# Kernel tuning notes

Measured on AMD Instinct MI355X. Metric: run time of the kernel, lower is better.

Reference implementation:

```python
import jax, jax.numpy as jnp
import numpy as np

NT = 256
T = 8192

def setup_inputs() -> dict:
    key = jax.random.key(0)
    k1, k2, k3, k4, k5 = jax.random.split(key, 5)
    emit = jax.random.normal(k1, (T, NT), dtype=jnp.float32)
    y = jax.random.randint(k2, (T,), 0, NT, dtype=jnp.int64)
    trans = jax.random.normal(k3, (NT, NT), dtype=jnp.float32)
    BOS = jax.random.normal(k4, (NT,), dtype=jnp.float32)
    EOS = jax.random.normal(k5, (NT,), dtype=jnp.float32)
    return {"emit": emit, "y": y, "trans": trans, "BOS": BOS, "EOS": EOS}

def _log_z(emit, trans, BOS):
    # alpha recurrence: alpha_new[j] = emit_i[j] + logsumexp_k(trans[k, j] + alpha[k])
    alpha0 = BOS + emit[0]
    def step(alpha, emit_i):
        alpha_new = emit_i + jax.nn.logsumexp(trans + alpha[:, None], axis=0)
        return alpha_new, None
    alpha, _ = jax.lax.scan(step, alpha0, emit[1:])
    return jax.nn.logsumexp(alpha)

def _gold_score(emit, y, trans, BOS, EOS):
    T_ = emit.shape[0]
    idx = jnp.arange(T_ - 1)
    s = BOS[y[0]]
    # faithful to original: emit[i, y[i]] for i in 0..T-2, plus trans[y[i], y[i+1]]
    s = s + jnp.sum(trans[y[:-1], y[1:]]) + jnp.sum(emit[idx, y[:-1]])
    s = s + EOS[y[-1]] + emit[-1, y[-1]]
    return s

def reference(emit, y, trans, BOS, EOS):
    logZ = _log_z(emit, trans, BOS)
    return logZ - _gold_score(emit, y, trans, BOS, EOS)
```

## Files before the change

kernel.cpp:

```cpp
#include <hip/hip_runtime.h>
#include <hip/hip_fp16.h>

#define TLEN 8192
#define NTS  256
#define CLEN 32
#define NCH  256
#define SLOT2 66048

typedef __bf16 bf16x8 __attribute__((ext_vector_type(8)));
typedef float  f32x4  __attribute__((ext_vector_type(4)));
union U128 { uint4 u; bf16x8 v; };
union U64  { uint2 u; long l; };

__device__ __forceinline__ unsigned f2bfu(float x) {
    unsigned u = __float_as_uint(x);
    return (u + 0x7fffu + ((u >> 16) & 1u)) >> 16;
}
__device__ __forceinline__ unsigned pk2(float lo, float hi) {
    return f2bfu(lo) | (f2bfu(hi) << 16);
}
__device__ __forceinline__ float bf2f(unsigned short h) {
    return __uint_as_float(((unsigned)h) << 16);
}
__device__ __forceinline__ unsigned pk4bf8(float a, float b, float c, float d) {
    int r = __builtin_amdgcn_cvt_pk_bf8_f32(a, b, 0, false);
    r = __builtin_amdgcn_cvt_pk_bf8_f32(c, d, r, true);
    return (unsigned)r;
}
__device__ __forceinline__ float dot8(uint4 a, const float* uq) {
    return bf2f((unsigned short)(a.x & 0xffffu)) * uq[0]
         + bf2f((unsigned short)(a.x >> 16))     * uq[1]
         + bf2f((unsigned short)(a.y & 0xffffu)) * uq[2]
         + bf2f((unsigned short)(a.y >> 16))     * uq[3]
         + bf2f((unsigned short)(a.z & 0xffffu)) * uq[4]
         + bf2f((unsigned short)(a.z >> 16))     * uq[5]
         + bf2f((unsigned short)(a.w & 0xffffu)) * uq[6]
         + bf2f((unsigned short)(a.w >> 16))     * uq[7];
}

__global__ __launch_bounds__(256, 2) void crf_phase1(
        const float* __restrict__ emit, const float* __restrict__ trans,
        char* __restrict__ outX) {
    __shared__ alignas(16) char qt8[65536];
    __shared__ alignas(16) char scr[4][1280];
    __shared__ alignas(16) float eld[2][NTS];

    const int t    = threadIdx.x;
    const int lane = t & 63;
    const int w    = t >> 6;
    const int gl   = lane >> 4;
    const int ln15 = lane & 15;
    const int c    = blockIdx.x >> 1;
    const int h    = blockIdx.x & 1;
    const int istart = (c == 0) ? 1 : CLEN * c;
    const int iend   = CLEN * c + CLEN;

    {
        const int ln = t & 15;
        for (int gk = 0; gk < 32; gk++) {
            float v[8];
            #pragma unroll
            for (int e = 0; e < 8; e++) v[e] = __expf(trans[(gk * 8 + e) * NTS + t]);
            uint2 u;
            u.x = pk4bf8(v[0], v[1], v[2], v[3]);
            u.y = pk4bf8(v[4], v[5], v[6], v[7]);
            const int p = (gk + 4 * ln + (ln >> 2)) & 31;
            *(uint2*)(qt8 + t * 256 + p * 8) = u;
        }
    }
    eld[istart & 1][t] = __expf(emit[istart * NTS + t]);

    int aoff[8];
    #pragma unroll
    for (int kf = 0; kf < 8; kf++) {
        const int p = (4 * kf + gl + 4 * ln15 + (ln15 >> 2)) & 31;
        aoff[kf] = ln15 * 256 + p * 8;
    }

    uint2 Bf[8][2];
    #pragma unroll
    for (int kf = 0; kf < 8; kf++)
        #pragma unroll
        for (int cb = 0; cb < 2; cb++) {
            uint2 bu; bu.x = 0u; bu.y = 0u;
            const int r_glob = 128 * h + 32 * w + cb * 16 + ln15;
            if ((r_glob >> 3) == kf * 4 + gl) {
                const int e = r_glob & 7;
                if (e < 4) bu.x = 0x3Cu << (8 * e);
                else       bu.y = 0x3Cu << (8 * (e - 4));
            }
            Bf[kf][cb] = bu;
        }
    float rs[2] = {0.f, 0.f};
    __syncthreads();

    char* const mysc = &scr[w][0];
    for (int i = istart; i < iend; ++i) {
        float enext = 0.f;
        if (i + 1 < iend) enext = emit[(i + 1) * NTS + t];

        f32x4 Cacc[16][2];
        #pragma unroll
        for (int jb = 0; jb < 16; jb++)
            #pragma unroll
            for (int cb = 0; cb < 2; cb++) Cacc[jb][cb] = f32x4{0.f, 0.f, 0.f, 0.f};

        #pragma unroll
        for (int jb = 0; jb < 16; jb++) {
            #pragma unroll
            for (int kf = 0; kf < 8; kf++) {
                U64 a; a.u = *(const uint2*)(qt8 + (aoff[kf] + jb * 4096));
                #pragma unroll
                for (int cb = 0; cb < 2; cb++) {
                    U64 b; b.u = Bf[kf][cb];
                    Cacc[jb][cb] = __builtin_amdgcn_mfma_f32_16x16x32_bf8_bf8(
                        a.l, b.l, Cacc[jb][cb], 0, 0, 0);
                }
            }
        }

        #pragma unroll
        for (int jb = 0; jb < 16; jb++) {
            float4 ev = *(const float4*)&eld[i & 1][jb * 16 + gl * 4];
            #pragma unroll
            for (int cb = 0; cb < 2; cb++) {
                Cacc[jb][cb][0] *= ev.x; Cacc[jb][cb][1] *= ev.y;
                Cacc[jb][cb][2] *= ev.z; Cacc[jb][cb][3] *= ev.w;
            }
        }
        float rn[2];
        #pragma unroll
        for (int cb = 0; cb < 2; cb++) {
            float m0 = Cacc[0][cb][0];
            #pragma unroll
            for (int jb = 0; jb < 16; jb++)
                #pragma unroll
                for (int rg = 0; rg < 4; rg++) m0 = fmaxf(m0, Cacc[jb][cb][rg]);
            m0 = fmaxf(m0, __shfl_xor(m0, 16));
            m0 = fmaxf(m0, __shfl_xor(m0, 32));
            rn[cb] = 1.0f / m0;
            rs[cb] += __logf(m0);
        }

        if (i == iend - 1) {
            __syncthreads();
            #pragma unroll
            for (int jb = 0; jb < 16; jb++)
                #pragma unroll
                for (int cb = 0; cb < 2; cb++) {
                    int rsl = w * 32 + cb * 16 + ln15;
                    #pragma unroll
                    for (int rg = 0; rg < 4; rg++) {
                        int j = jb * 16 + gl * 4 + rg;
                        *(unsigned short*)(qt8 + ((j * 128 + rsl) << 1)) =
                            (unsigned short)f2bfu(Cacc[jb][cb][rg] * rn[cb]);
                    }
                }
            __syncthreads();
            char* SO = outX + (size_t)(2 * c + h) * SLOT2;
            #pragma unroll
            for (int q = 0; q < 16; q++)
                *(uint4*)(SO + q * 4096 + t * 16) =
                    *(const uint4*)(qt8 + q * 4096 + t * 16);
            if (lane < 16) {
                #pragma unroll
                for (int cb = 0; cb < 2; cb++) {
                    int rsl = w * 32 + cb * 16 + lane;
                    *(float*)(SO + 65536 + rsl * 4) = rs[cb];
                }
            }
        } else {
            #pragma unroll
            for (int kf = 0; kf < 8; kf++) {
                #pragma unroll
                for (int jbb = 0; jbb < 2; jbb++) {
                    const int jb = 2 * kf + jbb;
                    #pragma unroll
                    for (int cb = 0; cb < 2; cb++) {
                        const int col = cb * 16 + ln15;
                        unsigned pk = pk4bf8(Cacc[jb][cb][0] * rn[cb],
                                             Cacc[jb][cb][1] * rn[cb],
                                             Cacc[jb][cb][2] * rn[cb],
                                             Cacc[jb][cb][3] * rn[cb]);
                        *(unsigned*)(mysc + col * 40 + jbb * 16 + gl * 4) = pk;
                    }
                }
                asm volatile("s_waitcnt lgkmcnt(0)" ::: "memory");
                __builtin_amdgcn_sched_barrier(0);
                #pragma unroll
                for (int cb = 0; cb < 2; cb++) {
                    const int col = cb * 16 + ln15;
                    Bf[kf][cb] = *(const uint2*)(mysc + col * 40 + gl * 8);
                }
                asm volatile("s_waitcnt lgkmcnt(0)" ::: "memory");
                __builtin_amdgcn_sched_barrier(0);
            }
            eld[(i + 1) & 1][t] = __expf(enext);
            __syncthreads();
        }
    }
}

__device__ __forceinline__ void combine_body(
        const char* __restrict__ inb, char* __restrict__ outb,
        int p, int h, char* qt, unsigned (*scr)[512],
        float* efac, float* smax,
        int t, int lane, int w, int gl, int ln15) {
    const char* SL0 = inb + (size_t)(4 * p + 2) * SLOT2;
    const char* SL1 = inb + (size_t)(4 * p + 3) * SLOT2;
    const char* SE  = inb + (size_t)(4 * p + h) * SLOT2;
    char* SO = outb + (size_t)(2 * p + h) * SLOT2;

    float sv = *(const float*)(((t < 128) ? SL0 : SL1) + 65536 + (t & 127) * 4);
    float m = sv;
    #pragma unroll
    for (int off = 32; off; off >>= 1) m = fmaxf(m, __shfl_xor(m, off));
    if (lane == 0) smax[w] = m;
    __syncthreads();
    const float sigma = fmaxf(fmaxf(smax[0], smax[1]), fmaxf(smax[2], smax[3]));
    efac[t] = __expf(sv - sigma);
    __syncthreads();

    for (int it = 0; it < 32; it++) {
        int off = it * 2048 + t * 8;
        int j = off >> 8, k = off & 255;
        const char* src = (k < 128) ? (SL0 + (size_t)(j * 128 + k) * 2)
                                    : (SL1 + (size_t)(j * 128 + (k - 128)) * 2);
        uint4 d = *(const uint4*)src;
        float4 e0 = *(const float4*)&efac[k];
        float4 e1 = *(const float4*)&efac[k + 4];
        float ef[8] = {e0.x, e0.y, e0.z, e0.w, e1.x, e1.y, e1.z, e1.w};
        unsigned wds[4] = {d.x, d.y, d.z, d.w};
        unsigned outw[4];
        #pragma unroll
        for (int wi = 0; wi < 4; wi++) {
            float lo = bf2f((unsigned short)(wds[wi] & 0xffffu)) * ef[2 * wi];
            float hi = bf2f((unsigned short)(wds[wi] >> 16)) * ef[2 * wi + 1];
            outw[wi] = pk2(lo, hi);
        }
        uint4 o; o.x = outw[0]; o.y = outw[1]; o.z = outw[2]; o.w = outw[3];
        *(uint4*)(qt + ((j * 512 + k * 2) ^ ((j & 7) << 4))) = o;
    }

    bf16x8 Bf[8][2];
    #pragma unroll
    for (int kf = 0; kf < 8; kf++) {
        #pragma unroll
        for (int p2 = 0; p2 < 2; p2++) {
            int kk = p2 * 16 + (lane >> 2);
            uint4 d = *(const uint4*)(SE + (size_t)(32 * kf + kk) * 256
                                      + w * 64 + (lane & 3) * 16);
            *(uint4*)((char*)&scr[w][0] + kk * 64 + (lane & 3) * 16) = d;
        }
        asm volatile("s_waitcnt lgkmcnt(0)" ::: "memory");
        __builtin_amdgcn_sched_barrier(0);
        #pragma unroll
        for (int cb = 0; cb < 2; cb++) {
            unsigned wd[4] = {0u, 0u, 0u, 0u};
            #pragma unroll
            for (int e = 0; e < 8; e++) {
                int kloc = gl * 8 + e;
                unsigned short hh = *(const unsigned short*)
                    ((const char*)&scr[w][0] + kloc * 64 + (cb * 16 + ln15) * 2);
                wd[e >> 1] |= ((unsigned)hh) << (16 * (e & 1));
            }
            U128 q; q.u.x = wd[0]; q.u.y = wd[1]; q.u.z = wd[2]; q.u.w = wd[3];
            Bf[kf][cb] = q.v;
        }
        asm volatile("s_waitcnt lgkmcnt(0)" ::: "memory");
        __builtin_amdgcn_sched_barrier(0);
    }
    __syncthreads();

    f32x4 Cacc[16][2];
    #pragma unroll
    for (int jb = 0; jb < 16; jb++)
        #pragma unroll
        for (int cb = 0; cb < 2; cb++) Cacc[jb][cb] = f32x4{0.f, 0.f, 0.f, 0.f};
    const int aswz = (lane & 7) << 4;
    #pragma unroll
    for (int jb = 0; jb < 16; jb++) {
        const int abase = (jb * 16 + ln15) * 512 + gl * 16;
        #pragma unroll
        for (int kf = 0; kf < 8; kf++) {
            U128 a; a.u = *(const uint4*)(qt + ((abase + kf * 64) ^ aswz));
            #pragma unroll
            for (int cb = 0; cb < 2; cb++)
                Cacc[jb][cb] = __builtin_amdgcn_mfma_f32_16x16x32_bf16(
                    a.v, Bf[kf][cb], Cacc[jb][cb], 0, 0, 0);
        }
    }

    float mx[2], rn[2];
    #pragma unroll
    for (int cb = 0; cb < 2; cb++) {
        float m0 = Cacc[0][cb][0];
        #pragma unroll
        for (int jb = 0; jb < 16; jb++)
            #pragma unroll
            for (int rg = 0; rg < 4; rg++) m0 = fmaxf(m0, Cacc[jb][cb][rg]);
        m0 = fmaxf(m0, __shfl_xor(m0, 16));
        m0 = fmaxf(m0, __shfl_xor(m0, 32));
        mx[cb] = m0; rn[cb] = 1.0f / m0;
    }

    __syncthreads();
    #pragma unroll
    for (int jb = 0; jb < 16; jb++)
        #pragma unroll
        for (int cb = 0; cb < 2; cb++) {
            int rsl = w * 32 + cb * 16 + ln15;
            #pragma unroll
            for (int rg = 0; rg < 4; rg++) {
                int j = jb * 16 + gl * 4 + rg;
                *(unsigned short*)(qt + ((j * 128 + rsl) << 1)) =
                    (unsigned short)f2bfu(Cacc[jb][cb][rg] * rn[cb]);
            }
        }
    __syncthreads();
    #pragma unroll
    for (int q = 0; q < 16; q++)
        *(uint4*)(SO + q * 4096 + t * 16) = *(const uint4*)(qt + q * 4096 + t * 16);
    if (lane < 16) {
        #pragma unroll
        for (int cb = 0; cb < 2; cb++) {
            int rsl = w * 32 + cb * 16 + lane;
            float se = *(const float*)(SE + 65536 + rsl * 4);
            *(float*)(SO + 65536 + rsl * 4) = se + sigma + __logf(mx[cb]);
        }
    }
}

__global__ __launch_bounds__(256, 1) void crf_combine2(
        const char* __restrict__ inb, char* __restrict__ outb) {
    __shared__ alignas(16) char qt[131072];
    __shared__ alignas(16) unsigned scr[4][512];
    __shared__ alignas(16) float efac[NTS];
    __shared__ float smax[4];
    const int t = threadIdx.x;
    combine_body(inb, outb, blockIdx.x >> 1, blockIdx.x & 1, qt, scr, efac, smax,
                 t, t & 63, t >> 6, (t & 63) >> 4, t & 15);
}

__global__ __launch_bounds__(512) void crf_chainfin16(
        const char* __restrict__ mats, const float* __restrict__ emit,
        const float* __restrict__ BOS, const int* __restrict__ y,
        const float* __restrict__ trans, const float* __restrict__ EOS,
        float* __restrict__ out) {
    __shared__ float red[8];
    __shared__ float smx[8];
    __shared__ alignas(16) float u[NTS];
    __shared__ float pu[NTS];
    const int t = threadIdx.x, lane = t & 63, wv = t >> 6;

    float s = 0.f;
    for (int i = t; i < TLEN - 1; i += 512) {
        int yi = y[i], yn = y[i + 1];
        s += trans[yi * NTS + yn] + emit[i * NTS + yi];
    }
    #pragma unroll
    for (int off = 32; off; off >>= 1) s += __shfl_down(s, off);
    if (lane == 0) red[wv] = s;

    float v0 = (t < NTS) ? (BOS[t] + emit[t]) : -INFINITY;
    float m = v0;
    #pragma unroll
    for (int off = 32; off; off >>= 1) m = fmaxf(m, __shfl_xor(m, off));
    if (lane == 0) smx[wv] = m;
    __syncthreads();
    const float m0 = fmaxf(fmaxf(smx[0], smx[1]), fmaxf(smx[2], smx[3]));
    float wreg = (t < NTS) ? __expf(v0 - m0) : 0.f;
    double W = (double)m0;
    __syncthreads();

    const int j2 = t & 255;
    const int hh = t >> 8;
    for (int c = 0; c < 16; ++c) {
        const char* M0 = mats + (size_t)(2 * c) * SLOT2;
        const char* M1 = M0 + SLOT2;

        const char* Mh = hh ? M1 : M0;
        const uint4* rowp = (const uint4*)(Mh + (size_t)j2 * 256);
        uint4 regs[16];
        #pragma unroll
        for (int q = 0; q < 16; q++) regs[q] = rowp[q];

        float sv = -INFINITY;
        if (t < NTS) sv = *(const float*)(((t < 128) ? M0 : M1) + 65536 + (t & 127) * 4);
        m = sv;
        #pragma unroll
        for (int off = 32; off; off >>= 1) m = fmaxf(m, __shfl_xor(m, off));
        if (lane == 0) smx[wv] = m;
        __syncthreads();
        const float sigma = fmaxf(fmaxf(smx[0], smx[1]), fmaxf(smx[2], smx[3]));
        if (t < NTS) u[t] = __expf(sv - sigma) * wreg;
        __syncthreads();

        const float* ub = u + hh * 128;
        float acc = 0.f;
        #pragma unroll
        for (int q = 0; q < 16; q++) acc += dot8(regs[q], ub + q * 8);
        if (hh == 1) pu[j2] = acc;
        __syncthreads();
        float v = -INFINITY;
        if (t < NTS) v = acc + pu[t];
        m = v;
        #pragma unroll
        for (int off = 32; off; off >>= 1) m = fmaxf(m, __shfl_xor(m, off));
        if (lane == 0) smx[wv] = m;
        __syncthreads();
        const float mstep = fmaxf(fmaxf(smx[0], smx[1]), fmaxf(smx[2], smx[3]));
        W += (double)(sigma + __logf(mstep));
        if (t < NTS) wreg = v * (1.0f / mstep);
        __syncthreads();
    }

    float ssum = (t < NTS) ? wreg : 0.f;
    #pragma unroll
    for (int off = 32; off; off >>= 1) ssum += __shfl_down(ssum, off);
    if (lane == 0) smx[wv] = ssum;
    __syncthreads();
    if (t == 0) {
        float S = smx[0] + smx[1] + smx[2] + smx[3];
        float logZ = (float)(W + (double)__logf(S));
        float gold = 0.f;
        #pragma unroll
        for (int k = 0; k < 8; k++) gold += red[k];
        int y0 = y[0], yl = y[TLEN - 1];
        gold += BOS[y0] + EOS[yl] + emit[(TLEN - 1) * NTS + yl];
        out[0] = logZ - gold;
    }
}

__global__ __launch_bounds__(256) void crf_prep(const float* __restrict__ trans,
                                                __half2* __restrict__ Qp) {
    int j = threadIdx.x, p = blockIdx.x;
    float a = __expf(trans[(2 * p) * NTS + j]);
    float b = __expf(trans[(2 * p + 1) * NTS + j]);
    Qp[p * NTS + j] = __floats2half2_rn(a, b);
}

__global__ __launch_bounds__(512) void crf_forward(
        const float* __restrict__ emit, const float* __restrict__ BOS,
        const __half2* __restrict__ Qp_g, float* __restrict__ logZ_out) {
    __shared__ __half2 Qp[128 * NTS];
    __shared__ alignas(16) float w[NTS];
    __shared__ float part[2][NTS];
    __shared__ float ebuf[2][NTS];
    __shared__ float wavemax[8];
    const int t = threadIdx.x, j = t & 255, q = t >> 8, lane = t & 63, wv = t >> 6;
    for (int idx = t; idx < 128 * NTS; idx += 512) Qp[idx] = Qp_g[idx];
    float anew = -INFINITY;
    if (t < NTS) anew = BOS[t] + emit[t];
    float ml = anew;
    #pragma unroll
    for (int off = 32; off; off >>= 1) ml = fmaxf(ml, __shfl_down(ml, off));
    if (lane == 0) wavemax[wv] = ml;
    __syncthreads();
    float mstep = fmaxf(fmaxf(wavemax[0], wavemax[1]), fmaxf(wavemax[2], wavemax[3]));
    double Macc = (double)mstep;
    if (t < NTS) w[t] = __expf(anew - mstep);
    float epre = 0.f;
    if (q == 1) epre = emit[NTS + j];
    __syncthreads();
    for (int i = 1; i < TLEN; ++i) {
        if (q == 1) ebuf[i & 1][j] = epre;
        float acc = 0.f;
        const __half2* qptr = Qp + (q * 64) * NTS + j;
        const float2* wptr = (const float2*)(w + q * 128);
        #pragma unroll 16
        for (int kk = 0; kk < 64; ++kk) {
            __half2 qv = qptr[kk * NTS];
            float2 wv2 = wptr[kk];
            acc += __low2float(qv) * wv2.x + __high2float(qv) * wv2.y;
        }
        part[q][j] = acc;
        if (q == 1 && (i + 1) < TLEN) epre = emit[(i + 1) * NTS + j];
        __syncthreads();
        float an = 0.f;
        ml = -INFINITY;
        if (t < NTS) {
            float vv = part[0][t] + part[1][t];
            an = ebuf[i & 1][t] + __logf(vv);
            ml = an;
        }
        #pragma unroll
        for (int off = 32; off; off >>= 1) ml = fmaxf(ml, __shfl_down(ml, off));
        if (lane == 0 && wv < 4) wavemax[wv] = ml;
        __syncthreads();
        mstep = fmaxf(fmaxf(wavemax[0], wavemax[1]), fmaxf(wavemax[2], wavemax[3]));
        Macc += (double)mstep;
        if (t < NTS) w[t] = __expf(an - mstep);
        __syncthreads();
    }
    float s = (t < NTS) ? w[t] : 0.f;
    #pragma unroll
    for (int off = 32; off; off >>= 1) s += __shfl_down(s, off);
    if (lane == 0 && wv < 4) wavemax[wv] = s;
    __syncthreads();
    if (t == 0) {
        float tot = wavemax[0] + wavemax[1] + wavemax[2] + wavemax[3];
        logZ_out[0] = (float)(Macc + (double)__logf(tot));
    }
}

__global__ __launch_bounds__(512) void crf_gold(
        const float* __restrict__ emit, const int* __restrict__ y,
        const float* __restrict__ trans, const float* __restrict__ BOS,
        const float* __restrict__ EOS, const float* __restrict__ logZ_ws,
        float* __restrict__ out) {
    __shared__ float red[8];
    int t = threadIdx.x;
    float s = 0.f;
    for (int i = t; i < TLEN - 1; i += 512) {
        int yi = y[i], yn = y[i + 1];
        s += trans[yi * NTS + yn] + emit[i * NTS + yi];
    }
    #pragma unroll
    for (int off = 32; off; off >>= 1) s += __shfl_down(s, off);
    if ((t & 63) == 0) red[t >> 6] = s;
    __syncthreads();
    if (t == 0) {
        float tot = 0.f;
        #pragma unroll
        for (int k2 = 0; k2 < 8; ++k2) tot += red[k2];
        int y0 = y[0], yl = y[TLEN - 1];
        tot += BOS[y0] + EOS[yl] + emit[(TLEN - 1) * NTS + yl];
        out[0] = logZ_ws[0] - tot;
    }
}

extern "C" void kernel_launch(void* const* d_in, const int* in_sizes, int n_in,
                              void* d_out, int out_size, void* d_ws, size_t ws_size,
                              hipStream_t stream) {
    const float* emit  = (const float*)d_in[0];
    const int*   y     = (const int*)d_in[1];
    const float* trans = (const float*)d_in[2];
    const float* BOS   = (const float*)d_in[3];
    const float* EOS   = (const float*)d_in[4];
    float* out = (float*)d_out;

    const size_t need = (size_t)(512 + 256) * SLOT2 + 256;
    if (ws_size >= need) {
        char* X = (char*)d_ws;
        char* Y = X + (size_t)512 * SLOT2;

        crf_phase1<<<2 * NCH, 256, 0, stream>>>(emit, trans, X);
        crf_combine2<<<256, 256, 0, stream>>>(X, Y);
        crf_combine2<<<128, 256, 0, stream>>>(Y, X);
        crf_combine2<<<64, 256, 0, stream>>>(X, Y);
        crf_combine2<<<32, 256, 0, stream>>>(Y, X);
        crf_chainfin16<<<1, 512, 0, stream>>>(X, emit, BOS, y, trans, EOS, out);
    } else {
        __half2* Qp = (__half2*)d_ws;
        float* logZ = (float*)((char*)d_ws + 128 * NTS * sizeof(__half2));
        crf_prep<<<128, 256, 0, stream>>>(trans, Qp);
        crf_forward<<<1, 512, 0, stream>>>(emit, BOS, Qp, logZ);
        crf_gold<<<1, 512, 0, stream>>>(emit, y, trans, BOS, EOS, logZ, out);
    }
}
```

Baseline: 409.2 us.

## Switch phase1 chain product to 16x16x128 scaled FP8 MFMA with K=128 fragments

Replaces the 16x16x32 bf8 MFMA sequence (8 k-steps per tile) with the gfx950 mfma_scale 16x16x128 f8f6f4 instruction, using 2 k-steps with 256-bit A/B fragments. The B-fragment repack through the per-wave scratch is changed to a swizzled 128-byte row layout read with 16-byte loads. This cuts the MFMA instruction count and issue overhead in the serial recurrence. In exchange it needs more registers per fragment, a larger scratch buffer and more complex K-index mapping, which could hurt occupancy or correctness.

Measured after the change: 394.0 us. 1.04x faster.

```diff
diff --git a/kernel.cpp b/kernel.cpp
--- a/kernel.cpp
+++ b/kernel.cpp
@@ -9,8 +9,10 @@
 
 typedef __bf16 bf16x8 __attribute__((ext_vector_type(8)));
 typedef float  f32x4  __attribute__((ext_vector_type(4)));
+typedef int    v8i    __attribute__((ext_vector_type(8)));
 union U128 { uint4 u; bf16x8 v; };
 union U64  { uint2 u; long l; };
+union U256 { unsigned u[8]; v8i v; };
 
 __device__ __forceinline__ unsigned f2bfu(float x) {
     unsigned u = __float_as_uint(x);
@@ -42,7 +44,7 @@
         const float* __restrict__ emit, const float* __restrict__ trans,
         char* __restrict__ outX) {
     __shared__ alignas(16) char qt8[65536];
-    __shared__ alignas(16) char scr[4][1280];
+    __shared__ alignas(16) char scr[4][2048];
     __shared__ alignas(16) float eld[2][NTS];
 
     const int t    = threadIdx.x;
@@ -70,28 +72,31 @@
     }
     eld[istart & 1][t] = __expf(emit[istart * NTS + t]);
 
-    int aoff[8];
-    #pragma unroll
-    for (int kf = 0; kf < 8; kf++) {
-        const int p = (4 * kf + gl + 4 * ln15 + (ln15 >> 2)) & 31;
-        aoff[kf] = ln15 * 256 + p * 8;
-    }
-
-    uint2 Bf[8][2];
-    #pragma unroll
-    for (int kf = 0; kf < 8; kf++)
+    int abase[2][4];
+    #pragma unroll
+    for (int kf2 = 0; kf2 < 2; kf2++)
+        #pragma unroll
+        for (int q = 0; q < 4; q++) {
+            const int gk = kf2 * 16 + gl * 4 + q;
+            const int p = (gk + 4 * ln15 + (ln15 >> 2)) & 31;
+            abase[kf2][q] = ln15 * 256 + p * 8;
+        }
+
+    v8i Bf[2][2];
+    #pragma unroll
+    for (int kf2 = 0; kf2 < 2; kf2++)
         #pragma unroll
         for (int cb = 0; cb < 2; cb++) {
-            uint2 bu; bu.x = 0u; bu.y = 0u;
+            U256 b;
+            #pragma unroll
+            for (int q = 0; q < 8; q++) b.u[q] = 0u;
             const int r_glob = 128 * h + 32 * w + cb * 16 + ln15;
-            if ((r_glob >> 3) == kf * 4 + gl) {
-                const int e = r_glob & 7;
-                if (e < 4) bu.x = 0x3Cu << (8 * e);
-                else       bu.y = 0x3Cu << (8 * (e - 4));
-            }
-            Bf[kf][cb] = bu;
+            const int e = r_glob - kf2 * 128 - gl * 32;
+            if (e >= 0 && e < 32) b.u[e >> 2] = 0x3Cu << (8 * (e & 3));
+            Bf[kf2][cb] = b.v;
         }
     float rs[2] = {0.f, 0.f};
+    const int swz = (ln15 & 7) << 4;
     __syncthreads();
 
     char* const mysc = &scr[w][0];
@@ -108,14 +113,20 @@
         #pragma unroll
         for (int jb = 0; jb < 16; jb++) {
             #pragma unroll
-            for (int kf = 0; kf < 8; kf++) {
-                U64 a; a.u = *(const uint2*)(qt8 + (aoff[kf] + jb * 4096));
+            for (int kf2 = 0; kf2 < 2; kf2++) {
+                U256 a;
                 #pragma unroll
-                for (int cb = 0; cb < 2; cb++) {
-                    U64 b; b.u = Bf[kf][cb];
-                    Cacc[jb][cb] = __builtin_amdgcn_mfma_f32_16x16x32_bf8_bf8(
-                        a.l, b.l, Cacc[jb][cb], 0, 0, 0);
+                for (int q = 0; q < 4; q++) {
+                    uint2 g = *(const uint2*)(qt8 + jb * 4096 + abase[kf2][q]);
+                    a.u[2 * q] = g.x; a.u[2 * q + 1] = g.y;
                 }
+                #pragma unroll
+                for (int cb = 0; cb < 2; cb++)
+                    Cacc[jb][cb] = __builtin_amdgcn_mfma_scale_f32_16x16x128_f8f6f4(
+                        a.v, Bf[kf2][cb], Cacc[jb][cb],
+                        1, 1,
+                        0, 0x7F,
+                        0, 0x7F);
             }
         }
 
@@ -171,29 +182,30 @@
             }
         } else {
             #pragma unroll
-            for (int kf = 0; kf < 8; kf++) {
+            for (int kf2 = 0; kf2 < 2; kf2++) {
                 #pragma unroll
-                for (int jbb = 0; jbb < 2; jbb++) {
-                    const int jb = 2 * kf + jbb;
+                for (int cb = 0; cb < 2; cb++) {
                     #pragma unroll
-                    for (int cb = 0; cb < 2; cb++) {
-                        const int col = cb * 16 + ln15;
+                    for (int jbl = 0; jbl < 8; jbl++) {
+                        const int jb = kf2 * 8 + jbl;
                         unsigned pk = pk4bf8(Cacc[jb][cb][0] * rn[cb],
                                              Cacc[jb][cb][1] * rn[cb],
                                              Cacc[jb][cb][2] * rn[cb],
                                              Cacc[jb][cb][3] * rn[cb]);
-                        *(unsigned*)(mysc + col * 40 + jbb * 16 + gl * 4) = pk;
+                        const int addr = ln15 * 128 + (((jbl * 16) ^ swz) + gl * 4);
+                        *(unsigned*)(mysc + addr) = pk;
                     }
+                    asm volatile("s_waitcnt lgkmcnt(0)" ::: "memory");
+                    __builtin_amdgcn_sched_barrier(0);
+                    uint4 r0 = *(const uint4*)(mysc + ln15 * 128 + ((gl * 32) ^ swz));
+                    uint4 r1 = *(const uint4*)(mysc + ln15 * 128 + ((gl * 32 + 16) ^ swz));
+                    U256 b;
+                    b.u[0] = r0.x; b.u[1] = r0.y; b.u[2] = r0.z; b.u[3] = r0.w;
+                    b.u[4] = r1.x; b.u[5] = r1.y; b.u[6] = r1.z; b.u[7] = r1.w;
+                    Bf[kf2][cb] = b.v;
+                    asm volatile("s_waitcnt lgkmcnt(0)" ::: "memory");
+                    __builtin_amdgcn_sched_barrier(0);
                 }
-                asm volatile("s_waitcnt lgkmcnt(0)" ::: "memory");
-                __builtin_amdgcn_sched_barrier(0);
-                #pragma unroll
-                for (int cb = 0; cb < 2; cb++) {
-                    const int col = cb * 16 + ln15;
-                    Bf[kf][cb] = *(const uint2*)(mysc + col * 40 + gl * 8);
-                }
-                asm volatile("s_waitcnt lgkmcnt(0)" ::: "memory");
-                __builtin_amdgcn_sched_barrier(0);
             }
             eld[(i + 1) & 1][t] = __expf(enext);
             __syncthreads();
```
